# Kernel tuning notes

Measured on AMD Instinct MI355X. Metric: run time of the kernel, lower is better.

Reference implementation:

```python
import jax, jax.numpy as jnp
import numpy as np

B, S, E, H, C = 64, 512, 768, 768, 9
Q_GCE = 0.7
TAU = 0.7
IGNORE = -100


def setup_inputs() -> dict:
    key = jax.random.key(0)
    k_h, k_w1, k_w2, k_lab, k_drop = jax.random.split(key, 5)
    hidden = jax.random.normal(k_h, (B, S, E), dtype=jnp.float32)
    W1 = jax.random.normal(k_w1, (E, H), dtype=jnp.float32) * (1.0 / np.sqrt(E))
    b1 = jnp.zeros((H,), dtype=jnp.float32)
    W2 = jax.random.normal(k_w2, (H, C), dtype=jnp.float32) * (1.0 / np.sqrt(H))
    b2 = jnp.zeros((C,), dtype=jnp.float32)
    labels = jax.random.randint(k_lab, (B, S), 0, C, dtype=jnp.int64 if jax.config.jax_enable_x64 else jnp.int32)
    drop = jax.random.uniform(k_drop, (B, S)) < 0.1
    labels = jnp.where(drop, IGNORE, labels)
    return {"hidden": hidden, "W1": W1, "b1": b1, "W2": W2, "b2": b2,
            "labels": labels, "epoch": 5}


def reference(hidden, W1, b1, W2, b2, labels, epoch):
    # head: Linear -> Tanh -> Linear (dropout is identity at eval)
    h = jnp.tanh(jnp.einsum('bse,eh->bsh', hidden, W1) + b1)
    logit = jnp.einsum('bsh,hc->bsc', h, W2) + b2
    probs = jax.nn.softmax(logit, axis=2)  # [B,S,C]

    mask = labels != IGNORE
    safe_labels = jnp.where(mask, labels, 0)
    # p_i = probs[i, labels[i]] gathered for every token
    p = jnp.take_along_axis(probs, safe_labels[..., None], axis=2)[..., 0]  # [B,S]
    # GCE weight: w=1 for epoch<=2, else 1 if p>tau else 0 (constant wrt grads)
    w = jnp.where(epoch <= 2, 1.0, jnp.where(p > TAU, 1.0, 0.0))
    w = jax.lax.stop_gradient(w) * mask.astype(probs.dtype)
    loss = jnp.sum(w * (1.0 - jnp.power(p, Q_GCE)) / Q_GCE)
    return probs, loss
```

## Files before the change

kernel.cpp:

```cpp
#include <hip/hip_runtime.h>
#include <hip/hip_bf16.h>
#include <stdint.h>

#define E_ 768
#define H_ 768
#define C_ 9
#define M_TOTAL 32768
#define BM_ 64

typedef __attribute__((ext_vector_type(8))) __bf16 bf16x8;
typedef __attribute__((ext_vector_type(4))) float f32x4;
typedef __attribute__((ext_vector_type(4))) int i32x4;

static_assert(sizeof(bf16x8) == 16, "bf16x8 must be 16B");

__device__ __forceinline__ unsigned short f2bf(float f) {
    __hip_bfloat16 h = __float2bfloat16(f);
    return __builtin_bit_cast(unsigned short, h);
}

__global__ void prep_kernel(const float* __restrict__ W1, const float* __restrict__ W2,
                            unsigned short* __restrict__ W1f, unsigned short* __restrict__ W2f,
                            float* __restrict__ loss_out)
{
    int b = blockIdx.x;
    int n = threadIdx.x;
    if (b < 768) {
        int k = b;
        float v = W1[k * H_ + n];
        int ntile = n >> 4;
        int t = k >> 5;
        int lane = (n & 15) + 16 * ((k >> 3) & 3);
        int j = k & 7;
        W1f[((ntile * 24 + t) * 64 + lane) * 8 + j] = f2bf(v);
    } else {
        for (int it = 0; it < 16; ++it) {
            int tid = it * 768 + n;
            int j    = tid & 7;
            int lane = (tid >> 3) & 63;
            int t    = tid >> 9;
            int cls  = lane & 15;
            int k = t * 32 + (lane >> 4) * 8 + j;
            W2f[tid] = (cls < C_) ? f2bf(W2[k * C_ + cls]) : (unsigned short)0;
        }
        if (n == 0) *loss_out = 0.0f;
    }
}

__launch_bounds__(512, 2)
__global__ void fused_head_kernel(const float* __restrict__ hidden,
                                  const unsigned short* __restrict__ W1f,
                                  const float* __restrict__ b1,
                                  const unsigned short* __restrict__ W2f,
                                  const float* __restrict__ b2,
                                  const int* __restrict__ labels,
                                  const int* __restrict__ epoch_p,
                                  float* __restrict__ probs,
                                  float* __restrict__ loss)
{
    __shared__ unsigned short Ast[2][8192];
    __shared__ unsigned short Hsh[12288];

    const int tid  = threadIdx.x;
    const int w    = tid >> 6;
    const int lane = tid & 63;
    const int tok0 = blockIdx.x * BM_;
    const int c16  = lane & 15;
    const int q    = lane >> 4;

    const int sg_jb = (w & 1) * 4;
    const float* gbase = hidden + (size_t)(tok0 + c16) * E_ + (w >> 1) * 32 + q * 8 + sg_jb;
    const int lbase = (w >> 1) * 2048 + lane * 8 + sg_jb;

    const unsigned short* Wp = W1f + (size_t)(w * 6 * 24) * 512 + lane * 8;

    {
        float4 v[4];
        #pragma unroll
        for (int u = 0; u < 4; ++u) v[u] = *(const float4*)(gbase + u * 16 * E_);
        #pragma unroll
        for (int u = 0; u < 4; ++u) {
            ushort4 p = { f2bf(v[u].x), f2bf(v[u].y), f2bf(v[u].z), f2bf(v[u].w) };
            *(ushort4*)(&Ast[0][lbase + u * 512]) = p;
        }
    }
    __syncthreads();

    const f32x4 zero4 = {0.0f, 0.0f, 0.0f, 0.0f};
    f32x4 acc[4][6];
    #pragma unroll
    for (int mt = 0; mt < 4; ++mt)
        #pragma unroll
        for (int nt = 0; nt < 6; ++nt) acc[mt][nt] = zero4;

#define KSTEP(Ab, t, s)                                                              \
    {                                                                                \
        const int tg = (s) * 4 + (t);                                                \
        bf16x8 bfr[6];                                                               \
        _Pragma("unroll")                                                            \
        for (int nt = 0; nt < 6; ++nt)                                               \
            bfr[nt] = __builtin_bit_cast(bf16x8,                                     \
                *(const i32x4*)(Wp + ((size_t)nt * 24 + tg) * 512));                 \
        _Pragma("unroll")                                                            \
        for (int mt = 0; mt < 4; ++mt) {                                             \
            bf16x8 af = __builtin_bit_cast(bf16x8,                                   \
                *(const i32x4*)(&(Ab)[((t) * 4 + mt) * 512 + lane * 8]));            \
            _Pragma("unroll")                                                        \
            for (int nt = 0; nt < 6; ++nt)                                           \
                acc[mt][nt] = __builtin_amdgcn_mfma_f32_16x16x32_bf16(               \
                    af, bfr[nt], acc[mt][nt], 0, 0, 0);                              \
        }                                                                            \
    }

    for (int s = 0; s < 6; ++s) {
        const unsigned short* Ab = Ast[s & 1];
        unsigned short* An = Ast[(s + 1) & 1];
        const bool pf = (s < 5);
        const float* gs = gbase + (s + 1) * 128;
        float4 v[4];
        if (pf) {
            #pragma unroll
            for (int u = 0; u < 4; ++u) v[u] = *(const float4*)(gs + u * 16 * E_);
        }
        KSTEP(Ab, 0, s)
        KSTEP(Ab, 1, s)
        KSTEP(Ab, 2, s)
        if (pf) {
            #pragma unroll
            for (int u = 0; u < 4; ++u) {
                ushort4 p = { f2bf(v[u].x), f2bf(v[u].y), f2bf(v[u].z), f2bf(v[u].w) };
                *(ushort4*)(&An[lbase + u * 512]) = p;
            }
        }
        KSTEP(Ab, 3, s)
        __syncthreads();
    }
#undef KSTEP

    f32x4 logit = zero4;
    const int myc = w >> 1;
    for (int c = 0; c < 4; ++c) {
        if (myc == c) {
            #pragma unroll
            for (int i = 0; i < 6; ++i) {
                int kloc = (w & 1) * 96 + i * 16 + c16;
                float b1v = b1[w * 96 + i * 16 + c16];
                int t2 = kloc >> 5;
                int q2 = (kloc >> 3) & 3;
                int j  = kloc & 7;
                #pragma unroll
                for (int mt = 0; mt < 4; ++mt) {
                    #pragma unroll
                    for (int r = 0; r < 4; ++r) {
                        float z = acc[mt][i][r] + b1v;
                        float e = exp2f(z * 2.8853900817779268f);
                        float th = 1.0f - 2.0f * __builtin_amdgcn_rcpf(e + 1.0f);
                        int lanep = (q * 4 + r) + 16 * q2;
                        Hsh[((t2 * 4 + mt) * 64 + lanep) * 8 + j] = f2bf(th);
                    }
                }
            }
        }
        __syncthreads();
        if (w < 4) {
            #pragma unroll
            for (int t2 = 0; t2 < 6; ++t2) {
                bf16x8 ha = __builtin_bit_cast(bf16x8, *(const i32x4*)(&Hsh[((t2 * 4 + w) * 64 + lane) * 8]));
                bf16x8 wb = __builtin_bit_cast(bf16x8, *(const i32x4*)(W2f + ((size_t)(c * 6 + t2) * 64 + lane) * 8));
                logit = __builtin_amdgcn_mfma_f32_16x16x32_bf16(ha, wb, logit, 0, 0, 0);
            }
        }
        __syncthreads();
    }

    if (w < 4) {
        const bool valid = (c16 < C_);
        const float b2v = valid ? b2[c16] : 0.0f;
        const int ep = epoch_p[0];
        float lsum = 0.0f;
        #pragma unroll
        for (int r = 0; r < 4; ++r) {
            float l = valid ? (logit[r] + b2v) : -3.0e38f;
            float m = l;
            #pragma unroll
            for (int d = 1; d < 16; d <<= 1)
                m = fmaxf(m, __shfl_xor(m, d, 64));
            float e = valid ? exp2f((l - m) * 1.44269504f) : 0.0f;
            float s = e;
            #pragma unroll
            for (int d = 1; d < 16; d <<= 1)
                s += __shfl_xor(s, d, 64);
            float p = e / s;
            int row = tok0 + w * 16 + q * 4 + r;
            if (valid) probs[(size_t)row * C_ + c16] = p;
            int lab = labels[row];
            if (valid && lab == c16) {
                float wgt = (ep <= 2) ? 1.0f : ((p > 0.7f) ? 1.0f : 0.0f);
                if (wgt > 0.0f)
                    lsum += (1.0f - exp2f(0.7f * log2f(p))) * (1.0f / 0.7f);
            }
        }
        #pragma unroll
        for (int d = 1; d < 64; d <<= 1)
            lsum += __shfl_xor(lsum, d, 64);
        if (lane == 0) atomicAdd(loss, lsum);
    }
}

extern "C" void kernel_launch(void* const* d_in, const int* in_sizes, int n_in,
                              void* d_out, int out_size, void* d_ws, size_t ws_size,
                              hipStream_t stream)
{
    const float* hidden = (const float*)d_in[0];
    const float* W1     = (const float*)d_in[1];
    const float* b1     = (const float*)d_in[2];
    const float* W2     = (const float*)d_in[3];
    const float* b2     = (const float*)d_in[4];
    const int*   labels = (const int*)d_in[5];
    const int*   epoch  = (const int*)d_in[6];

    float* probs = (float*)d_out;
    float* loss  = probs + (size_t)M_TOTAL * C_;

    unsigned short* W1f = (unsigned short*)d_ws;
    unsigned short* W2f = W1f + 48 * 24 * 512;

    prep_kernel<<<769, 768, 0, stream>>>(W1, W2, W1f, W2f, loss);
    fused_head_kernel<<<M_TOTAL / BM_, 512, 0, stream>>>(hidden, W1f, b1, W2f, b2,
                                                         labels, epoch, probs, loss);
}
```

Before: 250.2 us.

## Stage W1 fragments through double-buffered LDS via async global_load_lds

Reorders the prepared W1 fragment layout to be k-tile-major. The main GEMM loop now prefetches each k-slice of W1 into a double-buffered shared-memory area with direct global-to-LDS loads, instead of each wave reading its B fragments straight from global memory into registers. The aim is to hide global-load latency for the weight operand behind the MFMA work. In exchange it adds four block barriers per stage instead of one and raises shared-memory use to about 128KB. That likely stops two blocks fitting per CU and so cuts occupancy.

```diff
diff --git a/kernel.cpp b/kernel.cpp
--- a/kernel.cpp
+++ b/kernel.cpp
@@ -17,6 +17,12 @@
 __device__ __forceinline__ unsigned short f2bf(float f) {
     __hip_bfloat16 h = __float2bfloat16(f);
     return __builtin_bit_cast(unsigned short, h);
+}
+
+__device__ __forceinline__ void gl_lds16(const unsigned short* g, unsigned short* l) {
+    __builtin_amdgcn_global_load_lds(
+        (const __attribute__((address_space(1))) uint32_t*)g,
+        (__attribute__((address_space(3))) uint32_t*)l, 16, 0, 0);
 }
 
 __global__ void prep_kernel(const float* __restrict__ W1, const float* __restrict__ W2,
@@ -32,7 +38,7 @@
         int t = k >> 5;
         int lane = (n & 15) + 16 * ((k >> 3) & 3);
         int j = k & 7;
-        W1f[((ntile * 24 + t) * 64 + lane) * 8 + j] = f2bf(v);
+        W1f[((t * 48 + ntile) * 64 + lane) * 8 + j] = f2bf(v);
     } else {
         for (int it = 0; it < 16; ++it) {
             int tid = it * 768 + n;
@@ -58,8 +64,8 @@
                                   float* __restrict__ probs,
                                   float* __restrict__ loss)
 {
-    __shared__ unsigned short Ast[2][8192];
-    __shared__ unsigned short Hsh[12288];
+    __shared__ unsigned short Bsh[2][24576];
+    __shared__ unsigned short Asp[2][8192];
 
     const int tid  = threadIdx.x;
     const int w    = tid >> 6;
@@ -72,7 +78,7 @@
     const float* gbase = hidden + (size_t)(tok0 + c16) * E_ + (w >> 1) * 32 + q * 8 + sg_jb;
     const int lbase = (w >> 1) * 2048 + lane * 8 + sg_jb;
 
-    const unsigned short* Wp = W1f + (size_t)(w * 6 * 24) * 512 + lane * 8;
+    const unsigned short* Wg = W1f + (size_t)(w * 6) * 512 + lane * 8;
 
     {
         float4 v[4];
@@ -80,10 +86,13 @@
         for (int u = 0; u < 4; ++u) v[u] = *(const float4*)(gbase + u * 16 * E_);
         #pragma unroll
         for (int u = 0; u < 4; ++u) {
-            ushort4 p = { f2bf(v[u].x), f2bf(v[u].y), f2bf(v[u].z), f2bf(v[u].w) };
-            *(ushort4*)(&Ast[0][lbase + u * 512]) = p;
-        }
-    }
+            ushort4 pk = { f2bf(v[u].x), f2bf(v[u].y), f2bf(v[u].z), f2bf(v[u].w) };
+            *(ushort4*)(&Asp[0][lbase + u * 512]) = pk;
+        }
+    }
+    #pragma unroll
+    for (int i = 0; i < 6; ++i)
+        gl_lds16(Wg + (size_t)i * 512, &Bsh[0][(w * 6 + i) * 512]);
     __syncthreads();
 
     const f32x4 zero4 = {0.0f, 0.0f, 0.0f, 0.0f};
@@ -93,18 +102,17 @@
         #pragma unroll
         for (int nt = 0; nt < 6; ++nt) acc[mt][nt] = zero4;
 
-#define KSTEP(Ab, t, s)                                                              \
+#define CSTEP(Ab, Bb, x)                                                             \
     {                                                                                \
-        const int tg = (s) * 4 + (t);                                                \
         bf16x8 bfr[6];                                                               \
         _Pragma("unroll")                                                            \
         for (int nt = 0; nt < 6; ++nt)                                               \
             bfr[nt] = __builtin_bit_cast(bf16x8,                                     \
-                *(const i32x4*)(Wp + ((size_t)nt * 24 + tg) * 512));                 \
+                *(const i32x4*)(&(Bb)[((w * 6 + nt) * 64 + lane) * 8]));             \
         _Pragma("unroll")                                                            \
         for (int mt = 0; mt < 4; ++mt) {                                             \
             bf16x8 af = __builtin_bit_cast(bf16x8,                                   \
-                *(const i32x4*)(&(Ab)[((t) * 4 + mt) * 512 + lane * 8]));            \
+                *(const i32x4*)(&(Ab)[(((x) * 4 + mt) * 512) + lane * 8]));          \
             _Pragma("unroll")                                                        \
             for (int nt = 0; nt < 6; ++nt)                                           \
                 acc[mt][nt] = __builtin_amdgcn_mfma_f32_16x16x32_bf16(               \
@@ -112,31 +120,48 @@
         }                                                                            \
     }
 
-    for (int s = 0; s < 6; ++s) {
-        const unsigned short* Ab = Ast[s & 1];
-        unsigned short* An = Ast[(s + 1) & 1];
-        const bool pf = (s < 5);
-        const float* gs = gbase + (s + 1) * 128;
+#define BPREF(tn)                                                                    \
+    {                                                                                \
+        _Pragma("unroll")                                                            \
+        for (int i = 0; i < 6; ++i)                                                  \
+            gl_lds16(Wg + ((size_t)(tn) * 48 + i) * 512,                             \
+                     &Bsh[(tn) & 1][(w * 6 + i) * 512]);                             \
+    }
+
+    for (int p = 0; p < 6; ++p) {
+        const unsigned short* Ab = &Asp[p & 1][0];
+        unsigned short* An = &Asp[(p + 1) & 1][0];
+        const bool pf = (p < 5);
         float4 v[4];
+        BPREF(4 * p + 1)
         if (pf) {
             #pragma unroll
-            for (int u = 0; u < 4; ++u) v[u] = *(const float4*)(gs + u * 16 * E_);
-        }
-        KSTEP(Ab, 0, s)
-        KSTEP(Ab, 1, s)
-        KSTEP(Ab, 2, s)
+            for (int u = 0; u < 4; ++u)
+                v[u] = *(const float4*)(gbase + (p + 1) * 128 + u * 16 * E_);
+        }
+        CSTEP(Ab, Bsh[0], 0)
+        __syncthreads();
+        BPREF(4 * p + 2)
+        CSTEP(Ab, Bsh[1], 1)
+        __syncthreads();
+        BPREF(4 * p + 3)
         if (pf) {
             #pragma unroll
             for (int u = 0; u < 4; ++u) {
-                ushort4 p = { f2bf(v[u].x), f2bf(v[u].y), f2bf(v[u].z), f2bf(v[u].w) };
-                *(ushort4*)(&An[lbase + u * 512]) = p;
-            }
-        }
-        KSTEP(Ab, 3, s)
-        __syncthreads();
-    }
-#undef KSTEP
-
+                ushort4 pk = { f2bf(v[u].x), f2bf(v[u].y), f2bf(v[u].z), f2bf(v[u].w) };
+                *(ushort4*)(&An[lbase + u * 512]) = pk;
+            }
+        }
+        CSTEP(Ab, Bsh[0], 2)
+        __syncthreads();
+        if (p < 5) BPREF(4 * p + 4)
+        CSTEP(Ab, Bsh[1], 3)
+        __syncthreads();
+    }
+#undef CSTEP
+#undef BPREF
+
+    unsigned short* Hsh = &Bsh[0][0];
     f32x4 logit = zero4;
     const int myc = w >> 1;
     for (int c = 0; c < 4; ++c) {
@@ -223,7 +248,7 @@
     float* loss  = probs + (size_t)M_TOTAL * C_;
 
     unsigned short* W1f = (unsigned short*)d_ws;
-    unsigned short* W2f = W1f + 48 * 24 * 512;
+    unsigned short* W2f = W1f + 24 * 48 * 512;
 
     prep_kernel<<<769, 768, 0, stream>>>(W1, W2, W1f, W2f, loss);
     fused_head_kernel<<<M_TOTAL / BM_, 512, 0, stream>>>(hidden, W1f, b1, W2f, b2,
```

Measured after the change: 259.4 us. 1.04x slower.

## Load full hidden tile up front and split N across 16 waves

Applied to the files above, without the earlier changes.

Each block now uses 1024 threads (16 waves). Every wave covers 48 of the H columns instead of 96, which halves per-wave accumulators. The whole 64x768 hidden tile is converted to bf16 and staged into one large shared buffer before any MFMA work, using nontemporal loads, instead of the double-buffered k-slab pipeline. W1 fragments are software-prefetched into two register sets. Shared memory is reused for the tanh output. The aim is more waves for latency hiding and fewer syncs in the main loop, but hidden loads no longer overlap with compute, and the larger LDS footprint and the launch-bounds change may limit occupancy.

```diff
diff --git a/kernel.cpp b/kernel.cpp
--- a/kernel.cpp
+++ b/kernel.cpp
@@ -47,7 +47,7 @@
     }
 }
 
-__launch_bounds__(512, 2)
+__launch_bounds__(1024, 4)
 __global__ void fused_head_kernel(const float* __restrict__ hidden,
                                   const unsigned short* __restrict__ W1f,
                                   const float* __restrict__ b1,
@@ -58,8 +58,7 @@
                                   float* __restrict__ probs,
                                   float* __restrict__ loss)
 {
-    __shared__ unsigned short Ast[2][8192];
-    __shared__ unsigned short Hsh[12288];
+    __shared__ unsigned short Ash[24 * 4 * 512];
 
     const int tid  = threadIdx.x;
     const int w    = tid >> 6;
@@ -68,83 +67,93 @@
     const int c16  = lane & 15;
     const int q    = lane >> 4;
 
-    const int sg_jb = (w & 1) * 4;
-    const float* gbase = hidden + (size_t)(tok0 + c16) * E_ + (w >> 1) * 32 + q * 8 + sg_jb;
-    const int lbase = (w >> 1) * 2048 + lane * 8 + sg_jb;
-
-    const unsigned short* Wp = W1f + (size_t)(w * 6 * 24) * 512 + lane * 8;
-
     {
-        float4 v[4];
-        #pragma unroll
-        for (int u = 0; u < 4; ++u) v[u] = *(const float4*)(gbase + u * 16 * E_);
-        #pragma unroll
-        for (int u = 0; u < 4; ++u) {
-            ushort4 p = { f2bf(v[u].x), f2bf(v[u].y), f2bf(v[u].z), f2bf(v[u].w) };
-            *(ushort4*)(&Ast[0][lbase + u * 512]) = p;
+        const f32x4* hsrc = (const f32x4*)(hidden + (size_t)tok0 * E_);
+        #pragma unroll
+        for (int i = 0; i < 12; ++i) {
+            int slot = i * 1024 + tid;
+            int tk = slot / 192;
+            int fq = slot - tk * 192;
+            f32x4 v = __builtin_nontemporal_load(hsrc + (size_t)tk * 192 + fq);
+            int k = fq * 4;
+            int t = k >> 5, mt = tk >> 4;
+            int lnf = (tk & 15) + 16 * ((k >> 3) & 3);
+            int j = k & 7;
+            ushort4 pk = { f2bf(v[0]), f2bf(v[1]), f2bf(v[2]), f2bf(v[3]) };
+            *(ushort4*)(&Ash[((t * 4 + mt) * 64 + lnf) * 8 + j]) = pk;
         }
     }
     __syncthreads();
 
+    const unsigned short* Wp = W1f + (size_t)(w * 3 * 24) * 512 + lane * 8;
+
+    bf16x8 bA[3], bB[3];
+    #pragma unroll
+    for (int i = 0; i < 3; ++i)
+        bA[i] = __builtin_bit_cast(bf16x8, *(const i32x4*)(Wp + (i * 24 + 0) * 512));
+    #pragma unroll
+    for (int i = 0; i < 3; ++i)
+        bB[i] = __builtin_bit_cast(bf16x8, *(const i32x4*)(Wp + (i * 24 + 1) * 512));
+
     const f32x4 zero4 = {0.0f, 0.0f, 0.0f, 0.0f};
-    f32x4 acc[4][6];
+    f32x4 acc[4][3];
     #pragma unroll
     for (int mt = 0; mt < 4; ++mt)
         #pragma unroll
-        for (int nt = 0; nt < 6; ++nt) acc[mt][nt] = zero4;
-
-#define KSTEP(Ab, t, s)                                                              \
-    {                                                                                \
-        const int tg = (s) * 4 + (t);                                                \
-        bf16x8 bfr[6];                                                               \
-        _Pragma("unroll")                                                            \
-        for (int nt = 0; nt < 6; ++nt)                                               \
-            bfr[nt] = __builtin_bit_cast(bf16x8,                                     \
-                *(const i32x4*)(Wp + ((size_t)nt * 24 + tg) * 512));                 \
-        _Pragma("unroll")                                                            \
-        for (int mt = 0; mt < 4; ++mt) {                                             \
-            bf16x8 af = __builtin_bit_cast(bf16x8,                                   \
-                *(const i32x4*)(&(Ab)[((t) * 4 + mt) * 512 + lane * 8]));            \
-            _Pragma("unroll")                                                        \
-            for (int nt = 0; nt < 6; ++nt)                                           \
-                acc[mt][nt] = __builtin_amdgcn_mfma_f32_16x16x32_bf16(               \
-                    af, bfr[nt], acc[mt][nt], 0, 0, 0);                              \
-        }                                                                            \
-    }
-
-    for (int s = 0; s < 6; ++s) {
-        const unsigned short* Ab = Ast[s & 1];
-        unsigned short* An = Ast[(s + 1) & 1];
-        const bool pf = (s < 5);
-        const float* gs = gbase + (s + 1) * 128;
-        float4 v[4];
-        if (pf) {
-            #pragma unroll
-            for (int u = 0; u < 4; ++u) v[u] = *(const float4*)(gs + u * 16 * E_);
-        }
-        KSTEP(Ab, 0, s)
-        KSTEP(Ab, 1, s)
-        KSTEP(Ab, 2, s)
-        if (pf) {
-            #pragma unroll
-            for (int u = 0; u < 4; ++u) {
-                ushort4 p = { f2bf(v[u].x), f2bf(v[u].y), f2bf(v[u].z), f2bf(v[u].w) };
-                *(ushort4*)(&An[lbase + u * 512]) = p;
-            }
-        }
-        KSTEP(Ab, 3, s)
-        __syncthreads();
-    }
-#undef KSTEP
-
+        for (int nt = 0; nt < 3; ++nt) acc[mt][nt] = zero4;
+
+    #pragma unroll
+    for (int tt = 0; tt < 12; ++tt) {
+        {
+            bf16x8 af[4];
+            #pragma unroll
+            for (int mt = 0; mt < 4; ++mt)
+                af[mt] = __builtin_bit_cast(bf16x8,
+                    *(const i32x4*)(&Ash[(((2 * tt) * 4 + mt) * 64 + lane) * 8]));
+            #pragma unroll
+            for (int mt = 0; mt < 4; ++mt)
+                #pragma unroll
+                for (int nt = 0; nt < 3; ++nt)
+                    acc[mt][nt] = __builtin_amdgcn_mfma_f32_16x16x32_bf16(
+                        af[mt], bA[nt], acc[mt][nt], 0, 0, 0);
+        }
+        if (tt < 11) {
+            #pragma unroll
+            for (int i = 0; i < 3; ++i)
+                bA[i] = __builtin_bit_cast(bf16x8,
+                    *(const i32x4*)(Wp + (i * 24 + 2 * tt + 2) * 512));
+        }
+        {
+            bf16x8 af[4];
+            #pragma unroll
+            for (int mt = 0; mt < 4; ++mt)
+                af[mt] = __builtin_bit_cast(bf16x8,
+                    *(const i32x4*)(&Ash[(((2 * tt + 1) * 4 + mt) * 64 + lane) * 8]));
+            #pragma unroll
+            for (int mt = 0; mt < 4; ++mt)
+                #pragma unroll
+                for (int nt = 0; nt < 3; ++nt)
+                    acc[mt][nt] = __builtin_amdgcn_mfma_f32_16x16x32_bf16(
+                        af[mt], bB[nt], acc[mt][nt], 0, 0, 0);
+        }
+        if (tt < 11) {
+            #pragma unroll
+            for (int i = 0; i < 3; ++i)
+                bB[i] = __builtin_bit_cast(bf16x8,
+                    *(const i32x4*)(Wp + (i * 24 + 2 * tt + 3) * 512));
+        }
+    }
+    __syncthreads();
+
+    unsigned short* Hsh = &Ash[0];
     f32x4 logit = zero4;
-    const int myc = w >> 1;
+    const int myc = w >> 2;
     for (int c = 0; c < 4; ++c) {
         if (myc == c) {
             #pragma unroll
-            for (int i = 0; i < 6; ++i) {
-                int kloc = (w & 1) * 96 + i * 16 + c16;
-                float b1v = b1[w * 96 + i * 16 + c16];
+            for (int i = 0; i < 3; ++i) {
+                int kloc = (w & 3) * 48 + i * 16 + c16;
+                float b1v = b1[w * 48 + i * 16 + c16];
                 int t2 = kloc >> 5;
                 int q2 = (kloc >> 3) & 3;
                 int j  = kloc & 7;
@@ -226,6 +235,6 @@
     unsigned short* W2f = W1f + 48 * 24 * 512;
 
     prep_kernel<<<769, 768, 0, stream>>>(W1, W2, W1f, W2f, loss);
-    fused_head_kernel<<<M_TOTAL / BM_, 512, 0, stream>>>(hidden, W1f, b1, W2f, b2,
-                                                         labels, epoch, probs, loss);
-}
+    fused_head_kernel<<<M_TOTAL / BM_, 1024, 0, stream>>>(hidden, W1f, b1, W2f, b2,
+                                                          labels, epoch, probs, loss);
+}
```

Result: faster. 224.3 us (-10.3%).
